# Performance work log

Hardware: AMD Instinct MI355X
Metric: run time of the kernel (lower is better)

Reference implementation:

```python
import jax, jax.numpy as jnp
import numpy as np

NUM_RELS = 64
EDGES_PER_REL = 16384
N_NODES = 100000
IN_FEAT = 128
OUT_FEAT = 128
NUM_BASES = 16
E = NUM_RELS * EDGES_PER_REL


def setup_inputs() -> dict:
    key = jax.random.key(0)
    ks = jax.random.split(key, 8)
    feat = jax.random.normal(ks[0], (N_NODES, IN_FEAT), dtype=jnp.float32)
    weight = jax.random.normal(ks[1], (NUM_BASES, IN_FEAT, OUT_FEAT), dtype=jnp.float32) * 0.05
    w_comp = jax.random.normal(ks[2], (NUM_RELS, NUM_BASES), dtype=jnp.float32) * 0.3
    h_bias = jnp.zeros((OUT_FEAT,), dtype=jnp.float32)
    loop_weight = jax.random.normal(ks[3], (IN_FEAT, OUT_FEAT), dtype=jnp.float32) * 0.05
    norm = jax.random.uniform(ks[4], (E, 1), dtype=jnp.float32)
    src = jax.random.randint(ks[5], (E,), 0, N_NODES, dtype=jnp.int32).astype(jnp.int64)
    dst = jax.random.randint(ks[6], (E,), 0, N_NODES, dtype=jnp.int32).astype(jnp.int64)
    # edges are sorted by relation type with uniform per-relation sections
    etypes = jnp.repeat(jnp.arange(NUM_RELS, dtype=jnp.int64), EDGES_PER_REL)
    return {"feat": feat, "weight": weight, "w_comp": w_comp, "h_bias": h_bias,
            "loop_weight": loop_weight, "norm": norm, "src": src, "dst": dst,
            "etypes": etypes, "section": EDGES_PER_REL}


def reference(feat, weight, w_comp, h_bias, loop_weight, norm, src, dst, etypes, section):
    num_rels, num_bases = w_comp.shape
    n_nodes, in_feat = feat.shape
    out_feat = weight.shape[2]
    # basis composition: per-relation weights [R, in, out]
    W = jnp.matmul(w_comp, weight.reshape(num_bases, in_feat * out_feat))
    W = W.reshape(num_rels, in_feat, out_feat)
    # gather per-edge source features (edges sorted by relation, uniform sections)
    h_e = feat[src]                                   # [E, in]
    n_edges = h_e.shape[0]
    h_r = h_e.reshape(num_rels, section, in_feat)     # [R, e_r, in]
    msg = jnp.einsum('rei,rio->reo', h_r, W)          # grouped matmul
    msg = msg.reshape(n_edges, out_feat) * norm       # edge-norm scaling
    # scatter-sum aggregation to destination nodes
    node_repr = jax.ops.segment_sum(msg, dst, num_segments=n_nodes)
    node_repr = node_repr + h_bias + jnp.matmul(feat, loop_weight)
    return jax.nn.relu(node_repr)
```

## Files before the change

### kernel.cpp

```cpp
#include <hip/hip_runtime.h>

#define N_NODES 100000
#define N_PAD 100352
#define NBLK 392
#define IN_FEAT 128
#define OUT_FEAT 128
#define NUM_RELS 64
#define EDGES_PER_REL 16384
#define NUM_BASES 16
#define E_TOTAL (NUM_RELS * EDGES_PER_REL)

typedef __bf16 bf16x8 __attribute__((ext_vector_type(8)));
typedef float floatx4 __attribute__((ext_vector_type(4)));

__global__ __launch_bounds__(256) void compose_w_bf16_kernel(
    const float* __restrict__ weight, const float* __restrict__ w_comp,
    __bf16* __restrict__ Wp) {
  int idx = blockIdx.x * 256 + threadIdx.x;
  int r = idx >> 14;
  int off = idx & 16383;
  int j = off & 7, n = (off >> 3) & 127, kp = off >> 10;
  int k = kp * 8 + j;
  const float* wc = w_comp + r * NUM_BASES;
  float acc = 0.f;
#pragma unroll
  for (int b = 0; b < NUM_BASES; ++b)
    acc += wc[b] * weight[b * 16384 + k * 128 + n];
  Wp[idx] = (__bf16)acc;
}

__global__ __launch_bounds__(256) void pack_loop_w_kernel(
    const float* __restrict__ loop_w, __bf16* __restrict__ Lp) {
  int idx = blockIdx.x * 256 + threadIdx.x;
  int j = idx & 7, n = (idx >> 3) & 127, kp = idx >> 10;
  Lp[idx] = (__bf16)loop_w[(kp * 8 + j) * 128 + n];
}

__global__ __launch_bounds__(256) void compose_w_f32_kernel(
    const float* __restrict__ weight, const float* __restrict__ w_comp,
    float* __restrict__ W) {
  int idx = blockIdx.x * 256 + threadIdx.x;
  int r = idx >> 14;
  int io = idx & 16383;
  const float* wc = w_comp + r * NUM_BASES;
  float acc = 0.f;
#pragma unroll
  for (int b = 0; b < NUM_BASES; ++b)
    acc += wc[b] * weight[b * 16384 + io];
  W[idx] = acc;
}

__global__ __launch_bounds__(256) void init_out_mfma(
    const float* __restrict__ feat, const __bf16* __restrict__ Lp,
    const float* __restrict__ bias, float* __restrict__ out) {
  __shared__ __bf16 A_lds[64 * 136];
  int t = threadIdx.x;
  long base = (long)blockIdx.x * 64;
#pragma unroll
  for (int j = 0; j < 8; ++j) {
    int idx = t + j * 256;
    int e = idx >> 5, k4 = idx & 31;
    long n = base + e;
    float4 v = make_float4(0.f, 0.f, 0.f, 0.f);
    if (n < N_NODES) v = ((const float4*)feat)[n * 32 + k4];
    __bf16 tb[4] = {(__bf16)v.x, (__bf16)v.y, (__bf16)v.z, (__bf16)v.w};
    *(ushort4*)&A_lds[e * 136 + k4 * 4] = *(ushort4*)tb;
  }
  __syncthreads();

  int wave = t >> 6, lane = t & 63;
  int m16 = lane & 15, quad = lane >> 4;
  floatx4 acc[8];
#pragma unroll
  for (int nt = 0; nt < 8; ++nt) acc[nt] = (floatx4){0.f, 0.f, 0.f, 0.f};

  const __bf16* a_base = &A_lds[(wave * 16 + m16) * 136 + quad * 8];
#pragma unroll
  for (int ks = 0; ks < 4; ++ks) {
    bf16x8 a = *(const bf16x8*)(a_base + ks * 32);
    int kp = ks * 4 + quad;
#pragma unroll
    for (int nt = 0; nt < 8; ++nt) {
      bf16x8 b = *(const bf16x8*)(Lp + (kp * 128 + nt * 16 + m16) * 8);
      acc[nt] = __builtin_amdgcn_mfma_f32_16x16x32_bf16(a, b, acc[nt], 0, 0, 0);
    }
  }

  float bv[8];
#pragma unroll
  for (int nt = 0; nt < 8; ++nt) bv[nt] = bias[nt * 16 + m16];
#pragma unroll
  for (int r = 0; r < 4; ++r) {
    long n = base + wave * 16 + quad * 4 + r;
    if (n < N_NODES) {
#pragma unroll
      for (int nt = 0; nt < 8; ++nt)
        out[n * 128 + nt * 16 + m16] = acc[nt][r] + bv[nt];
    }
  }
}

__global__ __launch_bounds__(256) void zero_kernel(int* __restrict__ p) {
  p[blockIdx.x * 256 + threadIdx.x] = 0;
}

__global__ __launch_bounds__(256) void hist8_kernel(
    const int* __restrict__ dst, int* __restrict__ cnt8, int cshift) {
  int e = blockIdx.x * 256 + threadIdx.x;
  int c = e >> cshift;
  atomicAdd(&cnt8[c * N_PAD + dst[e]], 1);
}

__global__ __launch_bounds__(256) void scan1_kernel(
    const int* __restrict__ cnt, int* __restrict__ row,
    int* __restrict__ bsum) {
  __shared__ int s[256];
  int t = threadIdx.x;
  int idx = blockIdx.x * 256 + t;
  int v = cnt[idx];
  s[t] = v;
  __syncthreads();
  for (int o = 1; o < 256; o <<= 1) {
    int x = (t >= o) ? s[t - o] : 0;
    __syncthreads();
    s[t] += x;
    __syncthreads();
  }
  row[idx] = s[t] - v;
  if (t == 255) bsum[blockIdx.x] = s[t];
}

__global__ __launch_bounds__(512) void scan2_kernel(
    const int* __restrict__ bsum, int* __restrict__ boff) {
  __shared__ int s[512];
  int t = threadIdx.x;
  int v = (t < NBLK) ? bsum[blockIdx.x * NBLK + t] : 0;
  s[t] = v;
  __syncthreads();
  for (int o = 1; o < 512; o <<= 1) {
    int x = (t >= o) ? s[t - o] : 0;
    __syncthreads();
    s[t] += x;
    __syncthreads();
  }
  if (t < NBLK) boff[blockIdx.x * NBLK + t] = s[t] - v;
}

__global__ __launch_bounds__(256) void scan3_kernel(
    int* __restrict__ row, const int* __restrict__ boff,
    int* __restrict__ fill) {
  int idx = blockIdx.x * 256 + threadIdx.x;
  int v = row[idx] + boff[blockIdx.x];
  row[idx] = v;
  fill[idx] = v;
}

__global__ __launch_bounds__(256) void scatter_pos_kernel(
    const int* __restrict__ dst, int* __restrict__ fill8,
    int* __restrict__ pos, int cshift) {
  int e = blockIdx.x * 256 + threadIdx.x;
  int c = e >> cshift;
  pos[e] = atomicAdd(&fill8[c * N_PAD + dst[e]], 1);
}

__global__ __launch_bounds__(256) void edge_gemm_mfma(
    const float* __restrict__ feat, const __bf16* __restrict__ Wp,
    const float* __restrict__ norm, const int* __restrict__ src,
    const int* __restrict__ pos, unsigned short* __restrict__ msg, int e_lo) {
  __shared__ __bf16 A_lds[64 * 136];
  __shared__ int s_src[64];
  __shared__ int s_pos[64];
  __shared__ float s_norm[64];
  int t = threadIdx.x;
  long base = (long)e_lo + (long)blockIdx.x * 64;
  int rel = (int)(base >> 14);
  const __bf16* Wr = Wp + (long)rel * (IN_FEAT * OUT_FEAT);

  if (t < 64) {
    s_src[t] = src[base + t];
    s_pos[t] = pos[base + t];
    s_norm[t] = norm[base + t];
  }
  __syncthreads();
#pragma unroll
  for (int j = 0; j < 8; ++j) {
    int idx = t + j * 256;
    int e = idx >> 5, k4 = idx & 31;
    float4 v = ((const float4*)feat)[(long)s_src[e] * 32 + k4];
    __bf16 tb[4] = {(__bf16)v.x, (__bf16)v.y, (__bf16)v.z, (__bf16)v.w};
    *(ushort4*)&A_lds[e * 136 + k4 * 4] = *(ushort4*)tb;
  }
  __syncthreads();

  int wave = t >> 6, lane = t & 63;
  int m16 = lane & 15, quad = lane >> 4;
  floatx4 acc[8];
#pragma unroll
  for (int nt = 0; nt < 8; ++nt) acc[nt] = (floatx4){0.f, 0.f, 0.f, 0.f};

  const __bf16* a_base = &A_lds[(wave * 16 + m16) * 136 + quad * 8];
#pragma unroll
  for (int ks = 0; ks < 4; ++ks) {
    bf16x8 a = *(const bf16x8*)(a_base + ks * 32);
    int kp = ks * 4 + quad;
#pragma unroll
    for (int nt = 0; nt < 8; ++nt) {
      bf16x8 b = *(const bf16x8*)(Wr + (kp * 128 + nt * 16 + m16) * 8);
      acc[nt] = __builtin_amdgcn_mfma_f32_16x16x32_bf16(a, b, acc[nt], 0, 0, 0);
    }
  }

  __syncthreads();
#pragma unroll
  for (int r = 0; r < 4; ++r) {
    int erow = wave * 16 + quad * 4 + r;
    float nm = s_norm[erow];
#pragma unroll
    for (int nt = 0; nt < 8; ++nt)
      A_lds[erow * 136 + nt * 16 + m16] = (__bf16)(acc[nt][r] * nm);
  }
  __syncthreads();
#pragma unroll
  for (int it = 0; it < 4; ++it) {
    int idx = it * 256 + t;
    int row = idx >> 4, seg = idx & 15;
    uint4 v = *(const uint4*)&A_lds[row * 136 + seg * 8];
    *(uint4*)(msg + (long)s_pos[row] * 128 + seg * 8) = v;
  }
}

__global__ __launch_bounds__(256) void gather_csr_kernel(
    const unsigned short* __restrict__ msg, const int* __restrict__ rowc,
    float* __restrict__ out, int do_relu) {
  int wave = threadIdx.x >> 6, lane = threadIdx.x & 63;
  int n = blockIdx.x * 4 + wave;
  if (n >= N_NODES) return;
  int beg = rowc[n], end = rowc[n + 1];
  if (!do_relu && beg == end) return;
  int half = lane >> 5;
  int c4 = lane & 31;
  float s0 = 0.f, s1 = 0.f, s2 = 0.f, s3 = 0.f;
  for (int j = beg + half; j < end; j += 2) {
    uint2 m = *(const uint2*)(msg + (long)j * 128 + c4 * 4);
    s0 += __uint_as_float(m.x << 16);
    s1 += __uint_as_float(m.x & 0xFFFF0000u);
    s2 += __uint_as_float(m.y << 16);
    s3 += __uint_as_float(m.y & 0xFFFF0000u);
  }
  s0 += __shfl_down(s0, 32);
  s1 += __shfl_down(s1, 32);
  s2 += __shfl_down(s2, 32);
  s3 += __shfl_down(s3, 32);
  if (half == 0) {
    float4 o = ((float4*)out)[(long)n * 32 + c4];
    o.x += s0; o.y += s1; o.z += s2; o.w += s3;
    if (do_relu) {
      o.x = fmaxf(o.x, 0.f); o.y = fmaxf(o.y, 0.f);
      o.z = fmaxf(o.z, 0.f); o.w = fmaxf(o.w, 0.f);
    }
    ((float4*)out)[(long)n * 32 + c4] = o;
  }
}

__global__ __launch_bounds__(256) void init_out_f32_kernel(
    const float* __restrict__ feat, const float* __restrict__ loop_w,
    const float* __restrict__ bias, float* __restrict__ out) {
  __shared__ float4 A4[64][32];
  int t = threadIdx.x;
  long base = (long)blockIdx.x * 64;
#pragma unroll
  for (int j = 0; j < 8; ++j) {
    int idx = t + j * 256;
    int e = idx >> 5, k4 = idx & 31;
    long n = base + e;
    float4 v = make_float4(0.f, 0.f, 0.f, 0.f);
    if (n < N_NODES) v = ((const float4*)feat)[n * 32 + k4];
    A4[e][k4] = v;
  }
  __syncthreads();
  int og = t & 31, eg = t >> 5;
  float acc[8][4];
#pragma unroll
  for (int j = 0; j < 8; ++j)
#pragma unroll
    for (int d = 0; d < 4; ++d) acc[j][d] = 0.f;
  const float4* W4 = (const float4*)loop_w;
  for (int k4 = 0; k4 < 32; ++k4) {
    float4 a[8];
#pragma unroll
    for (int j = 0; j < 8; ++j) a[j] = A4[eg * 8 + j][k4];
#pragma unroll
    for (int d = 0; d < 4; ++d) {
      float4 w = W4[(k4 * 4 + d) * 32 + og];
#pragma unroll
      for (int j = 0; j < 8; ++j) {
        float av = ((const float*)&a[j])[d];
        acc[j][0] += av * w.x;
        acc[j][1] += av * w.y;
        acc[j][2] += av * w.z;
        acc[j][3] += av * w.w;
      }
    }
  }
  float4 b = ((const float4*)bias)[og];
#pragma unroll
  for (int j = 0; j < 8; ++j) {
    long n = base + eg * 8 + j;
    if (n < N_NODES) {
      float4 v = make_float4(acc[j][0] + b.x, acc[j][1] + b.y,
                             acc[j][2] + b.z, acc[j][3] + b.w);
      ((float4*)out)[n * 32 + og] = v;
    }
  }
}

__global__ __launch_bounds__(256) void edge_msg_atomic_kernel(
    const float* __restrict__ feat, const float* __restrict__ W,
    const float* __restrict__ norm, const int* __restrict__ src,
    const int* __restrict__ dst, float* __restrict__ out) {
  __shared__ float4 A4[64][32];
  __shared__ int s_src[64];
  __shared__ int s_dst[64];
  __shared__ float s_norm[64];
  int t = threadIdx.x;
  long base = (long)blockIdx.x * 64;
  int rel = blockIdx.x >> 8;
  const float4* Wr4 = (const float4*)(W + (long)rel * IN_FEAT * OUT_FEAT);
  if (t < 64) {
    s_src[t] = src[base + t];
    s_dst[t] = dst[base + t];
    s_norm[t] = norm[base + t];
  }
  __syncthreads();
#pragma unroll
  for (int j = 0; j < 8; ++j) {
    int idx = t + j * 256;
    int e = idx >> 5, k4 = idx & 31;
    A4[e][k4] = ((const float4*)feat)[(long)s_src[e] * 32 + k4];
  }
  __syncthreads();
  int og = t & 31, eg = t >> 5;
  float acc[8][4];
#pragma unroll
  for (int j = 0; j < 8; ++j)
#pragma unroll
    for (int d = 0; d < 4; ++d) acc[j][d] = 0.f;
  for (int k4 = 0; k4 < 32; ++k4) {
    float4 a[8];
#pragma unroll
    for (int j = 0; j < 8; ++j) a[j] = A4[eg * 8 + j][k4];
#pragma unroll
    for (int d = 0; d < 4; ++d) {
      float4 w = Wr4[(k4 * 4 + d) * 32 + og];
#pragma unroll
      for (int j = 0; j < 8; ++j) {
        float av = ((const float*)&a[j])[d];
        acc[j][0] += av * w.x;
        acc[j][1] += av * w.y;
        acc[j][2] += av * w.z;
        acc[j][3] += av * w.w;
      }
    }
  }
#pragma unroll
  for (int j = 0; j < 8; ++j) {
    int e = eg * 8 + j;
    float nm = s_norm[e];
    float* orow = out + (long)s_dst[e] * OUT_FEAT + og * 4;
#pragma unroll
    for (int d = 0; d < 4; ++d) atomicAdd(orow + d, acc[j][d] * nm);
  }
}

__global__ __launch_bounds__(256) void relu_kernel(float* __restrict__ out) {
  int idx = blockIdx.x * 256 + threadIdx.x;
  float4 v = ((const float4*)out)[idx];
  v.x = fmaxf(v.x, 0.f);
  v.y = fmaxf(v.y, 0.f);
  v.z = fmaxf(v.z, 0.f);
  v.w = fmaxf(v.w, 0.f);
  ((float4*)out)[idx] = v;
}

extern "C" void kernel_launch(void* const* d_in, const int* in_sizes, int n_in,
                              void* d_out, int out_size, void* d_ws, size_t ws_size,
                              hipStream_t stream) {
  const float* feat   = (const float*)d_in[0];
  const float* weight = (const float*)d_in[1];
  const float* w_comp = (const float*)d_in[2];
  const float* h_bias = (const float*)d_in[3];
  const float* loop_w = (const float*)d_in[4];
  const float* norm   = (const float*)d_in[5];
  const int*   src    = (const int*)d_in[6];
  const int*   dst    = (const int*)d_in[7];
  float* out = (float*)d_out;

  const size_t SZ_WP  = (size_t)NUM_RELS * IN_FEAT * OUT_FEAT * 2;
  const size_t SZ_LP  = (size_t)IN_FEAT * OUT_FEAT * 2;
  const size_t SZ_POS = (size_t)E_TOTAL * 4;

  int CH = 0;
  {
    const int cands[4] = {32, 16, 8, 4};
    for (int i = 0; i < 4 && CH == 0; ++i) {
      int ch = cands[i], nc = NUM_RELS / ch;
      size_t need = SZ_WP + SZ_LP + SZ_POS + 2 * (size_t)nc * N_PAD * 4 +
                    2 * (size_t)nc * NBLK * 4 +
                    (size_t)ch * EDGES_PER_REL * OUT_FEAT * 2;
      if (ws_size >= need) CH = ch;
    }
  }

  if (CH > 0) {
    const int NC = NUM_RELS / CH;
    const int chunk_edges = CH * EDGES_PER_REL;
    int cshift = 14;
    for (int x = CH; x > 1; x >>= 1) ++cshift;

    char* p = (char*)d_ws;
    __bf16* Wp = (__bf16*)p;                  p += SZ_WP;
    __bf16* Lp = (__bf16*)p;                  p += SZ_LP;
    int* pos  = (int*)p;                      p += SZ_POS;
    int* cnt8 = (int*)p;                      p += (size_t)NC * N_PAD * 4;
    int* row8 = (int*)p;                      p += (size_t)NC * N_PAD * 4;
    int* bsum = (int*)p;                      p += (size_t)NC * NBLK * 4;
    int* boff = (int*)p;                      p += (size_t)NC * NBLK * 4;
    unsigned short* msg = (unsigned short*)p;

    hipLaunchKernelGGL(pack_loop_w_kernel, dim3(16384 / 256), dim3(256), 0,
                       stream, loop_w, Lp);
    hipLaunchKernelGGL(init_out_mfma, dim3((N_NODES + 63) / 64), dim3(256), 0,
                       stream, feat, Lp, h_bias, out);
    hipLaunchKernelGGL(compose_w_bf16_kernel, dim3(NUM_RELS * 16384 / 256),
                       dim3(256), 0, stream, weight, w_comp, Wp);
    hipLaunchKernelGGL(zero_kernel, dim3(NC * NBLK), dim3(256), 0, stream, cnt8);
    hipLaunchKernelGGL(hist8_kernel, dim3(E_TOTAL / 256), dim3(256), 0, stream,
                       dst, cnt8, cshift);
    hipLaunchKernelGGL(scan1_kernel, dim3(NC * NBLK), dim3(256), 0, stream,
                       cnt8, row8, bsum);
    hipLaunchKernelGGL(scan2_kernel, dim3(NC), dim3(512), 0, stream, bsum, boff);
    hipLaunchKernelGGL(scan3_kernel, dim3(NC * NBLK), dim3(256), 0, stream,
                       row8, boff, cnt8);
    hipLaunchKernelGGL(scatter_pos_kernel, dim3(E_TOTAL / 256), dim3(256), 0,
                       stream, dst, cnt8, pos, cshift);

    for (int c = 0; c < NC; ++c) {
      hipLaunchKernelGGL(edge_gemm_mfma, dim3(chunk_edges / 64), dim3(256), 0,
                         stream, feat, Wp, norm, src, pos, msg,
                         c * chunk_edges);
      hipLaunchKernelGGL(gather_csr_kernel, dim3((N_NODES + 3) / 4), dim3(256),
                         0, stream, msg, row8 + (size_t)c * N_PAD, out,
                         (c == NC - 1) ? 1 : 0);
    }
  } else {
    float* W = (float*)d_ws;
    hipLaunchKernelGGL(init_out_f32_kernel, dim3((N_NODES + 63) / 64),
                       dim3(256), 0, stream, feat, loop_w, h_bias, out);
    hipLaunchKernelGGL(compose_w_f32_kernel, dim3(NUM_RELS * 16384 / 256),
                       dim3(256), 0, stream, weight, w_comp, W);
    hipLaunchKernelGGL(edge_msg_atomic_kernel, dim3(E_TOTAL / 64), dim3(256), 0,
                       stream, feat, W, norm, src, dst, out);
    hipLaunchKernelGGL(relu_kernel, dim3((N_NODES * OUT_FEAT / 4) / 256),
                       dim3(256), 0, stream, out);
  }
}
```

Before: 461.7 us.

## Pre-convert node features to bf16 and allow single-chunk processing

Adds a kernel that converts the fp32 feature matrix to bf16 once, so the edge GEMM and self-loop GEMM gather half as many bytes per edge row and skip per-edge conversion. The workspace selection now also tries a chunk size of 64 relations (one chunk), which cuts the per-chunk launches and gather passes when workspace allows. In exchange it costs an extra conversion pass over features and more workspace. If workspace is tight the bf16 buffer may push the choice to smaller chunks.

After: 446.1 us. 1.03x faster.

```diff
diff --git a/kernel.cpp b/kernel.cpp
--- a/kernel.cpp
+++ b/kernel.cpp
@@ -12,6 +12,16 @@
 
 typedef __bf16 bf16x8 __attribute__((ext_vector_type(8)));
 typedef float floatx4 __attribute__((ext_vector_type(4)));
+
+__global__ __launch_bounds__(256) void feat_to_bf16_kernel(
+    const float* __restrict__ feat, __bf16* __restrict__ fb) {
+  long i = ((long)blockIdx.x * 256 + threadIdx.x) * 8;
+  float4 a = *(const float4*)(feat + i);
+  float4 b = *(const float4*)(feat + i + 4);
+  __bf16 t8[8] = {(__bf16)a.x, (__bf16)a.y, (__bf16)a.z, (__bf16)a.w,
+                  (__bf16)b.x, (__bf16)b.y, (__bf16)b.z, (__bf16)b.w};
+  *(uint4*)(fb + i) = *(uint4*)t8;
+}
 
 __global__ __launch_bounds__(256) void compose_w_bf16_kernel(
     const float* __restrict__ weight, const float* __restrict__ w_comp,
@@ -51,20 +61,33 @@
 }
 
 __global__ __launch_bounds__(256) void init_out_mfma(
-    const float* __restrict__ feat, const __bf16* __restrict__ Lp,
-    const float* __restrict__ bias, float* __restrict__ out) {
+    const float* __restrict__ feat, const __bf16* __restrict__ featb,
+    const __bf16* __restrict__ Lp, const float* __restrict__ bias,
+    float* __restrict__ out) {
   __shared__ __bf16 A_lds[64 * 136];
   int t = threadIdx.x;
   long base = (long)blockIdx.x * 64;
-#pragma unroll
-  for (int j = 0; j < 8; ++j) {
-    int idx = t + j * 256;
-    int e = idx >> 5, k4 = idx & 31;
-    long n = base + e;
-    float4 v = make_float4(0.f, 0.f, 0.f, 0.f);
-    if (n < N_NODES) v = ((const float4*)feat)[n * 32 + k4];
-    __bf16 tb[4] = {(__bf16)v.x, (__bf16)v.y, (__bf16)v.z, (__bf16)v.w};
-    *(ushort4*)&A_lds[e * 136 + k4 * 4] = *(ushort4*)tb;
+  if (featb) {
+#pragma unroll
+    for (int j = 0; j < 4; ++j) {
+      int idx = t + j * 256;
+      int e = idx >> 4, seg = idx & 15;
+      long n = base + e;
+      uint4 v = make_uint4(0u, 0u, 0u, 0u);
+      if (n < N_NODES) v = ((const uint4*)featb)[n * 16 + seg];
+      *(uint4*)&A_lds[e * 136 + seg * 8] = v;
+    }
+  } else {
+#pragma unroll
+    for (int j = 0; j < 8; ++j) {
+      int idx = t + j * 256;
+      int e = idx >> 5, k4 = idx & 31;
+      long n = base + e;
+      float4 v = make_float4(0.f, 0.f, 0.f, 0.f);
+      if (n < N_NODES) v = ((const float4*)feat)[n * 32 + k4];
+      __bf16 tb[4] = {(__bf16)v.x, (__bf16)v.y, (__bf16)v.z, (__bf16)v.w};
+      *(ushort4*)&A_lds[e * 136 + k4 * 4] = *(ushort4*)tb;
+    }
   }
   __syncthreads();
 
@@ -164,9 +187,10 @@
 }
 
 __global__ __launch_bounds__(256) void edge_gemm_mfma(
-    const float* __restrict__ feat, const __bf16* __restrict__ Wp,
-    const float* __restrict__ norm, const int* __restrict__ src,
-    const int* __restrict__ pos, unsigned short* __restrict__ msg, int e_lo) {
+    const float* __restrict__ feat, const __bf16* __restrict__ featb,
+    const __bf16* __restrict__ Wp, const float* __restrict__ norm,
+    const int* __restrict__ src, const int* __restrict__ pos,
+    unsigned short* __restrict__ msg, int e_lo) {
   __shared__ __bf16 A_lds[64 * 136];
   __shared__ int s_src[64];
   __shared__ int s_pos[64];
@@ -182,13 +206,23 @@
     s_norm[t] = norm[base + t];
   }
   __syncthreads();
-#pragma unroll
-  for (int j = 0; j < 8; ++j) {
-    int idx = t + j * 256;
-    int e = idx >> 5, k4 = idx & 31;
-    float4 v = ((const float4*)feat)[(long)s_src[e] * 32 + k4];
-    __bf16 tb[4] = {(__bf16)v.x, (__bf16)v.y, (__bf16)v.z, (__bf16)v.w};
-    *(ushort4*)&A_lds[e * 136 + k4 * 4] = *(ushort4*)tb;
+  if (featb) {
+#pragma unroll
+    for (int j = 0; j < 4; ++j) {
+      int idx = t + j * 256;
+      int e = idx >> 4, seg = idx & 15;
+      uint4 v = ((const uint4*)featb)[(long)s_src[e] * 16 + seg];
+      *(uint4*)&A_lds[e * 136 + seg * 8] = v;
+    }
+  } else {
+#pragma unroll
+    for (int j = 0; j < 8; ++j) {
+      int idx = t + j * 256;
+      int e = idx >> 5, k4 = idx & 31;
+      float4 v = ((const float4*)feat)[(long)s_src[e] * 32 + k4];
+      __bf16 tb[4] = {(__bf16)v.x, (__bf16)v.y, (__bf16)v.z, (__bf16)v.w};
+      *(ushort4*)&A_lds[e * 136 + k4 * 4] = *(ushort4*)tb;
+    }
   }
   __syncthreads();
 
@@ -397,17 +431,19 @@
 
   const size_t SZ_WP  = (size_t)NUM_RELS * IN_FEAT * OUT_FEAT * 2;
   const size_t SZ_LP  = (size_t)IN_FEAT * OUT_FEAT * 2;
+  const size_t SZ_FB  = (size_t)N_NODES * IN_FEAT * 2;
   const size_t SZ_POS = (size_t)E_TOTAL * 4;
 
-  int CH = 0;
+  int CH = 0, FB = 0;
   {
-    const int cands[4] = {32, 16, 8, 4};
-    for (int i = 0; i < 4 && CH == 0; ++i) {
-      int ch = cands[i], nc = NUM_RELS / ch;
-      size_t need = SZ_WP + SZ_LP + SZ_POS + 2 * (size_t)nc * N_PAD * 4 +
-                    2 * (size_t)nc * NBLK * 4 +
+    const int chs[10] = {64, 32, 32, 16, 16, 8, 8, 4, 4, 0};
+    const int fbs[10] = { 1,  1,  0,  1,  0, 1, 0, 1, 0, 0};
+    for (int i = 0; i < 9 && CH == 0; ++i) {
+      int ch = chs[i], fb = fbs[i], nc = NUM_RELS / ch;
+      size_t need = SZ_WP + SZ_LP + (fb ? SZ_FB : 0) + SZ_POS +
+                    2 * (size_t)nc * N_PAD * 4 + 2 * (size_t)nc * NBLK * 4 +
                     (size_t)ch * EDGES_PER_REL * OUT_FEAT * 2;
-      if (ws_size >= need) CH = ch;
+      if (ws_size >= need) { CH = ch; FB = fb; }
     }
   }
 
@@ -420,6 +456,8 @@
     char* p = (char*)d_ws;
     __bf16* Wp = (__bf16*)p;                  p += SZ_WP;
     __bf16* Lp = (__bf16*)p;                  p += SZ_LP;
+    __bf16* featb = nullptr;
+    if (FB) { featb = (__bf16*)p;             p += SZ_FB; }
     int* pos  = (int*)p;                      p += SZ_POS;
     int* cnt8 = (int*)p;                      p += (size_t)NC * N_PAD * 4;
     int* row8 = (int*)p;                      p += (size_t)NC * N_PAD * 4;
@@ -427,10 +465,14 @@
     int* boff = (int*)p;                      p += (size_t)NC * NBLK * 4;
     unsigned short* msg = (unsigned short*)p;
 
+    if (FB)
+      hipLaunchKernelGGL(feat_to_bf16_kernel,
+                         dim3(N_NODES * IN_FEAT / 8 / 256), dim3(256), 0,
+                         stream, feat, featb);
     hipLaunchKernelGGL(pack_loop_w_kernel, dim3(16384 / 256), dim3(256), 0,
                        stream, loop_w, Lp);
     hipLaunchKernelGGL(init_out_mfma, dim3((N_NODES + 63) / 64), dim3(256), 0,
-                       stream, feat, Lp, h_bias, out);
+                       stream, feat, featb, Lp, h_bias, out);
     hipLaunchKernelGGL(compose_w_bf16_kernel, dim3(NUM_RELS * 16384 / 256),
                        dim3(256), 0, stream, weight, w_comp, Wp);
     hipLaunchKernelGGL(zero_kernel, dim3(NC * NBLK), dim3(256), 0, stream, cnt8);
@@ -446,7 +488,7 @@
 
     for (int c = 0; c < NC; ++c) {
       hipLaunchKernelGGL(edge_gemm_mfma, dim3(chunk_edges / 64), dim3(256), 0,
-                         stream, feat, Wp, norm, src, pos, msg,
+                         stream, feat, featb, Wp, norm, src, pos, msg,
                          c * chunk_edges);
       hipLaunchKernelGGL(gather_csr_kernel, dim3((N_NODES + 3) / 4), dim3(256),
                          0, stream, msg, row8 + (size_t)c * N_PAD, out,
```
